# Kernel tuning notes

Measured on AMD Instinct MI355X. Metric: run time of the kernel, lower is better.

The kernel has to match this reference:

```python
import jax, jax.numpy as jnp
import numpy as np

B, T, D = 2, 2048, 2048
NH, HD = 16, 128
Q_LAT, KV_LAT = 1024, 512
EPS = 1e-6
THETA = 10000.0


def setup_inputs() -> dict:
    key = jax.random.key(0)
    ks = jax.random.split(key, 8)
    x = jax.random.normal(ks[0], (B, T, D), dtype=jnp.float32)
    # causal additive mask, broadcast over batch/heads
    neg = jnp.finfo(jnp.float32).min
    causal = jnp.where(jnp.tril(jnp.ones((T, T), dtype=bool)), 0.0, neg)
    attn_mask = causal[None, None, :, :].astype(jnp.float32)
    s = lambda fan_in: 1.0 / np.sqrt(fan_in)
    q_a_w = jax.random.normal(ks[1], (Q_LAT, D), dtype=jnp.float32) * s(D)
    q_b_w = jax.random.normal(ks[2], (NH * HD, Q_LAT), dtype=jnp.float32) * s(Q_LAT)
    kv_a_w = jax.random.normal(ks[3], (KV_LAT, D), dtype=jnp.float32) * s(D)
    k_b_w = jax.random.normal(ks[4], (NH * HD, KV_LAT), dtype=jnp.float32) * s(KV_LAT)
    v_b_w = jax.random.normal(ks[5], (NH * HD, KV_LAT), dtype=jnp.float32) * s(KV_LAT)
    o_w = jax.random.normal(ks[6], (D, NH * HD), dtype=jnp.float32) * s(NH * HD)
    q_norm_w = jnp.ones((HD,), dtype=jnp.float32)
    k_norm_w = jnp.ones((HD,), dtype=jnp.float32)
    return dict(x=x, attn_mask=attn_mask, q_a_w=q_a_w, q_b_w=q_b_w, kv_a_w=kv_a_w,
                k_b_w=k_b_w, v_b_w=v_b_w, o_w=o_w, q_norm_w=q_norm_w, k_norm_w=k_norm_w)


def _rms_norm(x, w):
    var = jnp.mean(jnp.square(x), axis=-1, keepdims=True)
    return x * jax.lax.rsqrt(var + EPS) * w


def _rope_cache(t, hd, dtype):
    inv_freq = 1.0 / (THETA ** (jnp.arange(0, hd, 2, dtype=jnp.float32) / hd))
    freqs = jnp.arange(t, dtype=jnp.float32)[:, None] * inv_freq[None, :]  # [t, hd/2]
    emb = jnp.concatenate([freqs, freqs], axis=-1)  # [t, hd]
    return jnp.cos(emb).astype(dtype), jnp.sin(emb).astype(dtype)


def _rotate_half(x):
    h = x.shape[-1] // 2
    return jnp.concatenate([-x[..., h:], x[..., :h]], axis=-1)


def reference(x, attn_mask, q_a_w, q_b_w, kv_a_w, k_b_w, v_b_w, o_w, q_norm_w, k_norm_w):
    b, t, d = x.shape
    # low-rank projections (torch Linear: y = x @ W.T)
    q = (x @ q_a_w.T) @ q_b_w.T          # [b, t, nh*hd]
    kv = x @ kv_a_w.T                     # [b, t, kv_lat]
    k = kv @ k_b_w.T
    v = kv @ v_b_w.T
    q = q.reshape(b, t, NH, HD).transpose(0, 2, 1, 3)  # [b, nh, t, hd]
    k = k.reshape(b, t, NH, HD).transpose(0, 2, 1, 3)
    v = v.reshape(b, t, NH, HD).transpose(0, 2, 1, 3)
    # QK-norm over head dim
    q = _rms_norm(q, q_norm_w)
    k = _rms_norm(k, k_norm_w)
    # RoPE
    cos, sin = _rope_cache(t, HD, x.dtype)  # [t, hd]
    cos = cos[None, None, :, :]
    sin = sin[None, None, :, :]
    q = q * cos + _rotate_half(q) * sin
    k = k * cos + _rotate_half(k) * sin
    # attention
    sd = 1.0 / np.sqrt(HD)
    attn = jnp.einsum('bhqd,bhkd->bhqk', q, k) * sd + attn_mask
    attn = jax.nn.softmax(attn, axis=-1)
    out = jnp.einsum('bhqk,bhkd->bhqd', attn, v)
    out = out.transpose(0, 2, 1, 3).reshape(b, t, NH * HD)
    return out @ o_w.T
```

## Files before the change

### kernel.cpp

```cpp
#include <hip/hip_runtime.h>
#include <hip/hip_fp16.h>

typedef _Float16 f16;
typedef _Float16 f16x4 __attribute__((ext_vector_type(4)));
typedef _Float16 f16x8 __attribute__((ext_vector_type(8)));
typedef float f32x4 __attribute__((ext_vector_type(4)));

#define BT 4096
#define DMODEL 2048

__device__ __forceinline__ void gld16(const f16* g, f16* l) {
    __builtin_amdgcn_global_load_lds((const __attribute__((address_space(1))) void*)g,
                                     (__attribute__((address_space(3))) void*)l, 16, 0, 0);
}

struct Cvt7 {
    const float* s[7];
    f16* d[7];
    int off4[8];
};
__global__ __launch_bounds__(256) void k_cvt7(Cvt7 c) {
    int i = blockIdx.x * 256 + threadIdx.x;
    if (i >= c.off4[7]) return;
    int seg = 0;
#pragma unroll
    for (int k = 1; k < 7; ++k) seg += (i >= c.off4[k]);
    int j = i - c.off4[seg];
    float4 v = ((const float4*)c.s[seg])[j];
    f16x4 h;
    h[0] = (f16)v.x; h[1] = (f16)v.y; h[2] = (f16)v.z; h[3] = (f16)v.w;
    ((f16x4*)c.d[seg])[j] = h;
}

template <typename CT>
__global__ __launch_bounds__(256, 3) void k_gemm_bt(const f16* __restrict__ A,
                                                    const f16* __restrict__ Bm,
                                                    CT* __restrict__ C,
                                                    int M, int N, int K) {
    __shared__ __align__(16) char smem[16384];
    f16* Als = (f16*)smem;
    f16* Bls = (f16*)(smem + 8192);
    const int tid = threadIdx.x;
    const int w = tid >> 6, l = tid & 63;
    const int quad = l >> 4, ln = l & 15;
    const int m0 = blockIdx.y * 128, n0 = blockIdx.x * 128;
    const int wm = (w >> 1) * 64, wn = (w & 1) * 64;
    const int srow = l >> 2, scol = (l & 3) * 8;

    f32x4 acc[4][4];
#pragma unroll
    for (int i = 0; i < 4; ++i)
#pragma unroll
        for (int j = 0; j < 4; ++j)
#pragma unroll
            for (int r = 0; r < 4; ++r) acc[i][j][r] = 0.f;

    for (int k0 = 0; k0 < K; k0 += 32) {
#pragma unroll
        for (int c = 0; c < 2; ++c) {
            const int ch = w + 4 * c;
            gld16(A + (size_t)(m0 + ch * 16 + srow) * K + (k0 + scol), &Als[ch * 512]);
            gld16(Bm + (size_t)(n0 + ch * 16 + srow) * K + (k0 + scol), &Bls[ch * 512]);
        }
        __syncthreads();
        f16x8 af[4], bf[4];
#pragma unroll
        for (int i = 0; i < 4; ++i) af[i] = *(const f16x8*)&Als[(wm + 16 * i + ln) * 32 + quad * 8];
#pragma unroll
        for (int j = 0; j < 4; ++j) bf[j] = *(const f16x8*)&Bls[(wn + 16 * j + ln) * 32 + quad * 8];
#pragma unroll
        for (int i = 0; i < 4; ++i)
#pragma unroll
            for (int j = 0; j < 4; ++j)
                acc[i][j] = __builtin_amdgcn_mfma_f32_16x16x32_f16(af[i], bf[j], acc[i][j], 0, 0, 0);
        __syncthreads();
    }
    const int p_w = (w >> 1) ? 16 : 0;
#pragma unroll
    for (int i = 0; i < 4; ++i) {
        if constexpr (sizeof(CT) == 2) {
            f16* Cs = (f16*)smem;
#pragma unroll
            for (int j = 0; j < 4; ++j)
#pragma unroll
                for (int r = 0; r < 4; ++r)
                    Cs[(p_w + quad * 4 + r) * 136 + wn + 16 * j + ln] = (f16)acc[i][j][r];
            __syncthreads();
#pragma unroll
            for (int k2 = 0; k2 < 2; ++k2) {
                int idx = k2 * 256 + tid;
                int pr = idx >> 4, c = idx & 15;
                int rg = m0 + 16 * i + (pr & 15) + ((pr & 16) ? 64 : 0);
                *(f16x8*)&C[(size_t)rg * N + n0 + c * 8] = *(const f16x8*)&Cs[pr * 136 + c * 8];
            }
        } else {
            float* Cs = (float*)smem;
#pragma unroll
            for (int j = 0; j < 4; ++j)
#pragma unroll
                for (int r = 0; r < 4; ++r)
                    Cs[(p_w + quad * 4 + r) * 128 + wn + 16 * j + ln] = acc[i][j][r];
            __syncthreads();
#pragma unroll
            for (int k2 = 0; k2 < 4; ++k2) {
                int idx = k2 * 256 + tid;
                int pr = idx >> 5, c = idx & 31;
                int rg = m0 + 16 * i + (pr & 15) + ((pr & 16) ? 64 : 0);
                *(float4*)&C[(size_t)rg * N + n0 + c * 4] = *(const float4*)&Cs[pr * 128 + c * 4];
            }
        }
        __syncthreads();
    }
}

__global__ __launch_bounds__(256, 3) void k_gemm_dual(const f16* __restrict__ A,
                                                      const f16* __restrict__ B0,
                                                      const f16* __restrict__ B1,
                                                      f16* __restrict__ C0, f16* __restrict__ C1,
                                                      int K, int nsplit, int ld0, int ld1) {
    __shared__ __align__(16) char smem[16384];
    f16* Als = (f16*)smem;
    f16* Bls = (f16*)(smem + 8192);
    const int tid = threadIdx.x;
    const int w = tid >> 6, l = tid & 63;
    const int quad = l >> 4, ln = l & 15;
    const int m0 = blockIdx.y * 128, n0 = blockIdx.x * 128;
    const int wm = (w >> 1) * 64, wn = (w & 1) * 64;
    const int srow = l >> 2, scol = (l & 3) * 8;
    const f16* Bm = (n0 < nsplit) ? B0 + (size_t)n0 * K : B1 + (size_t)(n0 - nsplit) * K;

    f32x4 acc[4][4];
#pragma unroll
    for (int i = 0; i < 4; ++i)
#pragma unroll
        for (int j = 0; j < 4; ++j)
#pragma unroll
            for (int r = 0; r < 4; ++r) acc[i][j][r] = 0.f;

    for (int k0 = 0; k0 < K; k0 += 32) {
#pragma unroll
        for (int c = 0; c < 2; ++c) {
            const int ch = w + 4 * c;
            gld16(A + (size_t)(m0 + ch * 16 + srow) * K + (k0 + scol), &Als[ch * 512]);
            gld16(Bm + (size_t)(ch * 16 + srow) * K + (k0 + scol), &Bls[ch * 512]);
        }
        __syncthreads();
        f16x8 af[4], bf[4];
#pragma unroll
        for (int i = 0; i < 4; ++i) af[i] = *(const f16x8*)&Als[(wm + 16 * i + ln) * 32 + quad * 8];
#pragma unroll
        for (int j = 0; j < 4; ++j) bf[j] = *(const f16x8*)&Bls[(wn + 16 * j + ln) * 32 + quad * 8];
#pragma unroll
        for (int i = 0; i < 4; ++i)
#pragma unroll
            for (int j = 0; j < 4; ++j)
                acc[i][j] = __builtin_amdgcn_mfma_f32_16x16x32_f16(af[i], bf[j], acc[i][j], 0, 0, 0);
        __syncthreads();
    }
    f16* Cd; int ldc, cb;
    if (n0 < nsplit) { Cd = C0; ldc = ld0; cb = n0; }
    else             { Cd = C1; ldc = ld1; cb = n0 - nsplit; }
    const int p_w = (w >> 1) ? 16 : 0;
    f16* Cs = (f16*)smem;
#pragma unroll
    for (int i = 0; i < 4; ++i) {
#pragma unroll
        for (int j = 0; j < 4; ++j)
#pragma unroll
            for (int r = 0; r < 4; ++r)
                Cs[(p_w + quad * 4 + r) * 136 + wn + 16 * j + ln] = (f16)acc[i][j][r];
        __syncthreads();
#pragma unroll
        for (int k2 = 0; k2 < 2; ++k2) {
            int idx = k2 * 256 + tid;
            int pr = idx >> 4, c = idx & 15;
            int rg = m0 + 16 * i + (pr & 15) + ((pr & 16) ? 64 : 0);
            *(f16x8*)&Cd[(size_t)rg * ldc + cb + c * 8] = *(const f16x8*)&Cs[pr * 136 + c * 8];
        }
        __syncthreads();
    }
}

__global__ __launch_bounds__(256, 3) void k_gemm_kv(const f16* __restrict__ A,
                                                    const f16* __restrict__ B0,
                                                    const f16* __restrict__ B1,
                                                    f16* __restrict__ Ck, f16* __restrict__ Vt,
                                                    int K) {
    __shared__ __align__(16) char smem[16384];
    f16* Als = (f16*)smem;
    f16* Bls = (f16*)(smem + 8192);
    const int tid = threadIdx.x;
    const int w = tid >> 6, l = tid & 63;
    const int quad = l >> 4, ln = l & 15;
    const int m0 = blockIdx.y * 128, n0 = blockIdx.x * 128;
    const int wm = (w >> 1) * 64, wn = (w & 1) * 64;
    const int srow = l >> 2, scol = (l & 3) * 8;
    const f16* Bm = (n0 < 2048) ? B0 + (size_t)n0 * K : B1 + (size_t)(n0 - 2048) * K;

    f32x4 acc[4][4];
#pragma unroll
    for (int i = 0; i < 4; ++i)
#pragma unroll
        for (int j = 0; j < 4; ++j)
#pragma unroll
            for (int r = 0; r < 4; ++r) acc[i][j][r] = 0.f;

    for (int k0 = 0; k0 < K; k0 += 32) {
#pragma unroll
        for (int c = 0; c < 2; ++c) {
            const int ch = w + 4 * c;
            gld16(A + (size_t)(m0 + ch * 16 + srow) * K + (k0 + scol), &Als[ch * 512]);
            gld16(Bm + (size_t)(ch * 16 + srow) * K + (k0 + scol), &Bls[ch * 512]);
        }
        __syncthreads();
        f16x8 af[4], bf[4];
#pragma unroll
        for (int i = 0; i < 4; ++i) af[i] = *(const f16x8*)&Als[(wm + 16 * i + ln) * 32 + quad * 8];
#pragma unroll
        for (int j = 0; j < 4; ++j) bf[j] = *(const f16x8*)&Bls[(wn + 16 * j + ln) * 32 + quad * 8];
#pragma unroll
        for (int i = 0; i < 4; ++i)
#pragma unroll
            for (int j = 0; j < 4; ++j)
                acc[i][j] = __builtin_amdgcn_mfma_f32_16x16x32_f16(af[i], bf[j], acc[i][j], 0, 0, 0);
        __syncthreads();
    }
    const int p_w = (w >> 1) ? 16 : 0;
    f16* Cs = (f16*)smem;
    const int bb = m0 >> 11;
    const int tb = m0 & 2047;
#pragma unroll
    for (int i = 0; i < 4; ++i) {
#pragma unroll
        for (int j = 0; j < 4; ++j)
#pragma unroll
            for (int r = 0; r < 4; ++r)
                Cs[(p_w + quad * 4 + r) * 136 + wn + 16 * j + ln] = (f16)acc[i][j][r];
        __syncthreads();
        if (n0 < 2048) {
#pragma unroll
            for (int k2 = 0; k2 < 2; ++k2) {
                int idx = k2 * 256 + tid;
                int pr = idx >> 4, c = idx & 15;
                int rg = m0 + 16 * i + (pr & 15) + ((pr & 16) ? 64 : 0);
                *(f16x8*)&Ck[(size_t)rg * 2048 + n0 + c * 8] = *(const f16x8*)&Cs[pr * 136 + c * 8];
            }
        } else {
#pragma unroll
            for (int it = 0; it < 2; ++it) {
                int idx = it * 256 + tid;
                int d = idx & 127, tc = (idx >> 7) & 1, g = idx >> 8;
                f16x8 v;
#pragma unroll
                for (int k = 0; k < 8; ++k) v[k] = Cs[(g * 16 + tc * 8 + k) * 136 + d];
                int t = tb + 16 * i + g * 64 + tc * 8;
                *(f16x8*)&Vt[((size_t)(bb * 2048 + (n0 - 2048) + d)) * 2048 + t] = v;
            }
        }
        __syncthreads();
    }
}

__global__ __launch_bounds__(256) void k_norm_rope(f16* __restrict__ q, f16* __restrict__ k,
                                                   const float* __restrict__ qw,
                                                   const float* __restrict__ kw) {
    const int gw = blockIdx.x * 4 + (threadIdx.x >> 6);
    const int l = threadIdx.x & 63;
    const int which = gw >> 16;
    const int rh = gw & 65535;
    const int row = rh >> 4, h = rh & 15;
    f16* p = which ? k : q;
    const float* wp = which ? kw : qw;
    const float scale = which ? 1.0f : 0.08838834764831843f;
    const size_t base = (size_t)row * DMODEL + h * 128;
    float xa = (float)p[base + l];
    float xb = (float)p[base + 64 + l];
    float ss = xa * xa + xb * xb;
#pragma unroll
    for (int off = 32; off > 0; off >>= 1) ss += __shfl_xor(ss, off);
    const float rms = rsqrtf(ss * (1.0f / 128.0f) + 1e-6f);
    const float na = xa * rms * wp[l];
    const float nb = xb * rms * wp[64 + l];
    const int t = row & 2047;
    const float freq = __expf((float)l * -0.1439115683121279f);
    const float ang = (float)t * freq;
    const float c = cosf(ang), s = sinf(ang);
    p[base + l]      = (f16)((na * c - nb * s) * scale);
    p[base + 64 + l] = (f16)((nb * c + na * s) * scale);
}

__global__ __launch_bounds__(256, 3) void k_flash(const f16* __restrict__ Q, const f16* __restrict__ K,
                                                  const f16* __restrict__ Vt, f16* __restrict__ O) {
    __shared__ f16 Kl[64 * 136];
    __shared__ f16 Vl[128 * 72];
    const int h = blockIdx.x, b = blockIdx.y, mt = 31 - blockIdx.z;
    const int tid = threadIdx.x, w = tid >> 6, l64 = tid & 63;
    const int quad = l64 >> 4, ln = l64 & 15;

    f16x8 qf[4];
    {
        const int tq = mt * 64 + w * 16 + ln;
        const f16* qp = Q + (size_t)(b * 2048 + tq) * DMODEL + h * 128 + quad * 8;
#pragma unroll
        for (int kc = 0; kc < 4; ++kc) qf[kc] = *(const f16x8*)(qp + kc * 32);
    }
    f32x4 oacc[8];
#pragma unroll
    for (int ot = 0; ot < 8; ++ot)
#pragma unroll
        for (int r = 0; r < 4; ++r) oacc[ot][r] = 0.f;
    float m_r = -INFINITY, l_r = 0.f;

    const f16* kbase = K + (size_t)(b * 2048) * DMODEL + h * 128;
    const f16* vbase = Vt + (size_t)(b * 2048 + h * 128) * 2048;

    f16x8 kr[4], vr[4];
#pragma unroll
    for (int c = 0; c < 4; ++c) {
        int idx = c * 256 + tid;
        kr[c] = *(const f16x8*)(kbase + (size_t)(idx >> 4) * DMODEL + (idx & 15) * 8);
        vr[c] = *(const f16x8*)(vbase + (size_t)(idx >> 3) * 2048 + (idx & 7) * 8);
    }

    for (int j = 0; j <= mt; ++j) {
        __syncthreads();
#pragma unroll
        for (int c = 0; c < 4; ++c) {
            int idx = c * 256 + tid;
            *(f16x8*)&Kl[(idx >> 4) * 136 + (idx & 15) * 8] = kr[c];
            *(f16x8*)&Vl[(idx >> 3) * 72 + (idx & 7) * 8] = vr[c];
        }
        __syncthreads();
        if (j < mt) {
#pragma unroll
            for (int c = 0; c < 4; ++c) {
                int idx = c * 256 + tid;
                kr[c] = *(const f16x8*)(kbase + (size_t)((j + 1) * 64 + (idx >> 4)) * DMODEL + (idx & 15) * 8);
                vr[c] = *(const f16x8*)(vbase + (size_t)(idx >> 3) * 2048 + (j + 1) * 64 + (idx & 7) * 8);
            }
        }
        f32x4 sacc[4];
#pragma unroll
        for (int nt = 0; nt < 4; ++nt)
#pragma unroll
            for (int r = 0; r < 4; ++r) sacc[nt][r] = 0.f;
#pragma unroll
        for (int nt = 0; nt < 4; ++nt)
#pragma unroll
            for (int kc = 0; kc < 4; ++kc) {
                f16x8 kf = *(const f16x8*)&Kl[(nt * 16 + ln) * 136 + kc * 32 + quad * 8];
                sacc[nt] = __builtin_amdgcn_mfma_f32_16x16x32_f16(kf, qf[kc], sacc[nt], 0, 0, 0);
            }
        if (j == mt) {
#pragma unroll
            for (int nt = 0; nt < 4; ++nt)
#pragma unroll
                for (int r = 0; r < 4; ++r)
                    if (nt * 16 + quad * 4 + r > w * 16 + ln) sacc[nt][r] = -INFINITY;
        }
        float mx = -INFINITY;
#pragma unroll
        for (int nt = 0; nt < 4; ++nt)
#pragma unroll
            for (int r = 0; r < 4; ++r) mx = fmaxf(mx, sacc[nt][r]);
        mx = fmaxf(mx, __shfl_xor(mx, 16));
        mx = fmaxf(mx, __shfl_xor(mx, 32));
        const float mn = fmaxf(m_r, mx);
        const float alpha = __expf(m_r - mn);
        m_r = mn;
        f16x4 pa[4];
        float s0 = 0.f;
#pragma unroll
        for (int nt = 0; nt < 4; ++nt)
#pragma unroll
            for (int r = 0; r < 4; ++r) {
                float pv = __expf(sacc[nt][r] - mn);
                s0 += pv;
                pa[nt][r] = (f16)pv;
            }
        s0 += __shfl_xor(s0, 16);
        s0 += __shfl_xor(s0, 32);
        l_r = l_r * alpha + s0;
        float ar[4];
#pragma unroll
        for (int r = 0; r < 4; ++r) ar[r] = __shfl(alpha, (l64 & 48) | (quad * 4 + r));
#pragma unroll
        for (int ot = 0; ot < 8; ++ot)
#pragma unroll
            for (int r = 0; r < 4; ++r) oacc[ot][r] *= ar[r];
#pragma unroll
        for (int nt = 0; nt < 4; ++nt)
#pragma unroll
            for (int ot = 0; ot < 8; ++ot) {
                f16x4 vf = *(const f16x4*)&Vl[(ot * 16 + ln) * 72 + nt * 16 + quad * 4];
                oacc[ot] = __builtin_amdgcn_mfma_f32_16x16x16f16(pa[nt], vf, oacc[ot], 0, 0, 0);
            }
    }
    const float inv = 1.0f / l_r;
    float ivr[4];
#pragma unroll
    for (int r = 0; r < 4; ++r) ivr[r] = __shfl(inv, (l64 & 48) | (quad * 4 + r));
    __syncthreads();
#pragma unroll
    for (int ot = 0; ot < 8; ++ot)
#pragma unroll
        for (int r = 0; r < 4; ++r)
            Kl[(w * 16 + quad * 4 + r) * 136 + ot * 16 + ln] = (f16)(oacc[ot][r] * ivr[r]);
    __syncthreads();
#pragma unroll
    for (int c = 0; c < 4; ++c) {
        int idx = c * 256 + tid;
        int row = idx >> 4, col8 = (idx & 15) * 8;
        *(f16x8*)&O[(size_t)(b * 2048 + mt * 64 + row) * DMODEL + h * 128 + col8] =
            *(const f16x8*)&Kl[row * 136 + col8];
    }
}

extern "C" void kernel_launch(void* const* d_in, const int* in_sizes, int n_in,
                              void* d_out, int out_size, void* d_ws, size_t ws_size,
                              hipStream_t stream) {
    const float* x    = (const float*)d_in[0];
    const float* qaw  = (const float*)d_in[2];
    const float* qbw  = (const float*)d_in[3];
    const float* kvaw = (const float*)d_in[4];
    const float* kbw  = (const float*)d_in[5];
    const float* vbw  = (const float*)d_in[6];
    const float* ow   = (const float*)d_in[7];
    const float* qnw  = (const float*)d_in[8];
    const float* knw  = (const float*)d_in[9];
    float* out = (float*)d_out;

    char* p = (char*)d_ws;
    auto alloc = [&](size_t elems) { f16* r = (f16*)p; p += elems * sizeof(f16); return r; };
    f16* xb   = alloc((size_t)BT * 2048);
    f16* wo   = alloc((size_t)2048 * 2048);
    f16* wqa  = alloc((size_t)1024 * 2048);
    f16* wqb  = alloc((size_t)2048 * 1024);
    f16* wkva = alloc((size_t)512 * 2048);
    f16* wkb  = alloc((size_t)2048 * 512);
    f16* wvb  = alloc((size_t)2048 * 512);
    f16* qlat = alloc((size_t)BT * 1024);
    f16* kvb  = alloc((size_t)BT * 512);
    f16* qpre = alloc((size_t)BT * 2048);
    f16* kpre = alloc((size_t)BT * 2048);
    f16* vt   = xb;
    f16* attn = wqa;

    Cvt7 c;
    c.s[0] = x;    c.d[0] = xb;
    c.s[1] = qaw;  c.d[1] = wqa;
    c.s[2] = qbw;  c.d[2] = wqb;
    c.s[3] = kvaw; c.d[3] = wkva;
    c.s[4] = kbw;  c.d[4] = wkb;
    c.s[5] = vbw;  c.d[5] = wvb;
    c.s[6] = ow;   c.d[6] = wo;
    int sz4[7] = {BT * 2048 / 4, 1024 * 2048 / 4, 2048 * 1024 / 4, 512 * 2048 / 4,
                  2048 * 512 / 4, 2048 * 512 / 4, 2048 * 2048 / 4};
    c.off4[0] = 0;
    for (int i = 0; i < 7; ++i) c.off4[i + 1] = c.off4[i] + sz4[i];
    k_cvt7<<<(c.off4[7] + 255) / 256, 256, 0, stream>>>(c);

    dim3 blk(256);
    k_gemm_dual<<<dim3(1536 / 128, BT / 128), blk, 0, stream>>>(xb, wqa, wkva, qlat, kvb, 2048, 1024, 1024, 512);
    k_gemm_bt<f16><<<dim3(2048 / 128, BT / 128), blk, 0, stream>>>(qlat, wqb, qpre, BT, 2048, 1024);
    k_gemm_kv<<<dim3(4096 / 128, BT / 128), blk, 0, stream>>>(kvb, wkb, wvb, kpre, vt, 512);
    k_norm_rope<<<32768, 256, 0, stream>>>(qpre, kpre, qnw, knw);
    k_flash<<<dim3(16, 2, 32), 256, 0, stream>>>(qpre, kpre, vt, attn);
    k_gemm_bt<float><<<dim3(2048 / 128, BT / 128), blk, 0, stream>>>(attn, wo, out, BT, 2048, 2048);
}
```

Before: 405.6 us.

## Add pipelined 8-wave output GEMM and lazy softmax rescaling in flash attention

Replaces the output projection GEMM with a new 512-thread, 128x256-tile kernel that double-buffers K slices through direct global-to-LDS loads, using explicit waitcnt/barrier scheduling and priority raising around the MFMA blocks. Separately, the flash attention loop now skips updating the running max and rescaling the accumulator unless the new tile max exceeds the old one by more than 8. This avoids per-iteration exp and accumulator multiplies. The lazy rescale lets unnormalized probabilities grow up to e^8 before being stored in fp16, which stays within range but adds precision risk. The new GEMM trades occupancy for larger tiles and overlap.

```diff
diff --git a/kernel.cpp b/kernel.cpp
--- a/kernel.cpp
+++ b/kernel.cpp
@@ -261,6 +261,107 @@
     }
 }
 
+__global__ __launch_bounds__(512, 2) void k_gemm8f(const f16* __restrict__ A,
+                                                   const f16* __restrict__ B0,
+                                                   float* __restrict__ C0,
+                                                   int K, int ld0) {
+    __shared__ __align__(16) f16 lds[49152];
+    const int tid = threadIdx.x;
+    const int w = tid >> 6, l = tid & 63;
+    const int wm = w >> 2, wn = w & 3;
+    const int quad = l >> 4, ln = l & 15;
+    const int m0 = blockIdx.y * 128, n0 = blockIdx.x * 256;
+
+    const f16* Bp = B0 + (size_t)n0 * K;
+
+    const f16* ag  = A + (size_t)(m0 + w * 16 + (l >> 2)) * K + (l & 3) * 8;
+    const f16* bg0 = Bp + (size_t)(w * 16 + (l >> 2)) * K + (l & 3) * 8;
+    const f16* bg1 = bg0 + (size_t)128 * K;
+    f16* al = &lds[w * 512];
+    f16* bl = &lds[4096 + w * 512];
+
+#define STAGE8(buf_, kc_, t_)                          \
+    {                                                  \
+        const int off_ = ((buf_) * 2 + (kc_)) * 12288; \
+        const int g_ = (t_) * 64 + (kc_) * 32;         \
+        gld16(ag + g_, al + off_);                     \
+        gld16(bg0 + g_, bl + off_);                    \
+        gld16(bg1 + g_, bl + off_ + 4096);             \
+    }
+
+    f32x4 acc[4][4];
+#pragma unroll
+    for (int i = 0; i < 4; ++i)
+#pragma unroll
+        for (int j = 0; j < 4; ++j)
+#pragma unroll
+            for (int r = 0; r < 4; ++r) acc[i][j][r] = 0.f;
+
+    const int nt = K >> 6;
+    STAGE8(0, 0, 0);
+    STAGE8(0, 1, 0);
+    STAGE8(1, 0, 1);
+    asm volatile("s_waitcnt vmcnt(3)" ::: "memory");
+    __builtin_amdgcn_s_barrier();
+    asm volatile("s_waitcnt lgkmcnt(0)" ::: "memory");
+
+    for (int t = 0; t < nt; ++t) {
+        const int buf = t & 1;
+#pragma unroll
+        for (int kc = 0; kc < 2; ++kc) {
+            const f16* Ah = &lds[(buf * 2 + kc) * 12288];
+            const f16* Bh = Ah + 4096;
+            f16x8 a[4], b[4];
+#pragma unroll
+            for (int i = 0; i < 4; ++i)
+                a[i] = *(const f16x8*)&Ah[(wm * 64 + i * 16 + ln) * 32 + quad * 8];
+#pragma unroll
+            for (int j = 0; j < 4; ++j)
+                b[j] = *(const f16x8*)&Bh[(wn * 64 + j * 16 + ln) * 32 + quad * 8];
+            if (kc == 0) {
+                if (t + 1 < nt) STAGE8(buf ^ 1, 1, t + 1);
+            } else {
+                if (t + 2 < nt) STAGE8(buf, 0, t + 2);
+            }
+            __builtin_amdgcn_s_barrier();
+            asm volatile("s_waitcnt lgkmcnt(0)" ::: "memory");
+            __builtin_amdgcn_s_setprio(1);
+#pragma unroll
+            for (int i = 0; i < 4; ++i)
+#pragma unroll
+                for (int j = 0; j < 4; ++j)
+                    acc[i][j] = __builtin_amdgcn_mfma_f32_16x16x32_f16(a[i], b[j], acc[i][j], 0, 0, 0);
+            __builtin_amdgcn_s_setprio(0);
+            if (kc == 1 && t + 1 < nt) {
+                if (t + 2 < nt) asm volatile("s_waitcnt vmcnt(3)" ::: "memory");
+                else            asm volatile("s_waitcnt vmcnt(0)" ::: "memory");
+            }
+            __builtin_amdgcn_s_barrier();
+        }
+    }
+#undef STAGE8
+
+    const int p = (wm ? 16 : 0) + quad * 4;
+    float* Cs = (float*)lds;
+#pragma unroll
+    for (int i = 0; i < 4; ++i) {
+        __syncthreads();
+#pragma unroll
+        for (int j = 0; j < 4; ++j)
+#pragma unroll
+            for (int r = 0; r < 4; ++r)
+                Cs[(p + r) * 260 + wn * 64 + j * 16 + ln] = acc[i][j][r];
+        __syncthreads();
+#pragma unroll
+        for (int rr = 0; rr < 4; ++rr) {
+            int idx = rr * 512 + tid;
+            int row = idx >> 6, c4 = idx & 63;
+            int rg = m0 + i * 16 + (row & 15) + ((row & 16) ? 64 : 0);
+            *(float4*)&C0[(size_t)rg * ld0 + n0 + c4 * 4] = *(const float4*)&Cs[row * 260 + c4 * 4];
+        }
+    }
+}
+
 __global__ __launch_bounds__(256) void k_norm_rope(f16* __restrict__ q, f16* __restrict__ k,
                                                    const float* __restrict__ qw,
                                                    const float* __restrict__ kw) {
@@ -365,8 +466,9 @@
             for (int r = 0; r < 4; ++r) mx = fmaxf(mx, sacc[nt][r]);
         mx = fmaxf(mx, __shfl_xor(mx, 16));
         mx = fmaxf(mx, __shfl_xor(mx, 32));
-        const float mn = fmaxf(m_r, mx);
-        const float alpha = __expf(m_r - mn);
+        const bool grow = (mx > m_r + 8.f);
+        const float mn = grow ? fmaxf(m_r, mx) : m_r;
+        const float alpha = grow ? __expf(m_r - mn) : 1.f;
         m_r = mn;
         f16x4 pa[4];
         float s0 = 0.f;
@@ -381,13 +483,15 @@
         s0 += __shfl_xor(s0, 16);
         s0 += __shfl_xor(s0, 32);
         l_r = l_r * alpha + s0;
-        float ar[4];
-#pragma unroll
-        for (int r = 0; r < 4; ++r) ar[r] = __shfl(alpha, (l64 & 48) | (quad * 4 + r));
-#pragma unroll
-        for (int ot = 0; ot < 8; ++ot)
-#pragma unroll
-            for (int r = 0; r < 4; ++r) oacc[ot][r] *= ar[r];
+        if (__ballot(grow)) {
+            float ar[4];
+#pragma unroll
+            for (int r = 0; r < 4; ++r) ar[r] = __shfl(alpha, (l64 & 48) | (quad * 4 + r));
+#pragma unroll
+            for (int ot = 0; ot < 8; ++ot)
+#pragma unroll
+                for (int r = 0; r < 4; ++r) oacc[ot][r] *= ar[r];
+        }
 #pragma unroll
         for (int nt = 0; nt < 4; ++nt)
 #pragma unroll
@@ -466,5 +570,5 @@
     k_gemm_kv<<<dim3(4096 / 128, BT / 128), blk, 0, stream>>>(kvb, wkb, wvb, kpre, vt, 512);
     k_norm_rope<<<32768, 256, 0, stream>>>(qpre, kpre, qnw, knw);
     k_flash<<<dim3(16, 2, 32), 256, 0, stream>>>(qpre, kpre, vt, attn);
-    k_gemm_bt<float><<<dim3(2048 / 128, BT / 128), blk, 0, stream>>>(attn, wo, out, BT, 2048, 2048);
-}
+    k_gemm8f<<<dim3(2048 / 256, BT / 128), 512, 0, stream>>>(attn, wo, out, 2048, 2048);
+}
```

Measured after the change: 394.2 us. 2.8% less time.
